# Performance work log

Measured on AMD Instinct MI355X. Metric: run time of the kernel, lower is better.

The kernel has to match this reference:

```python
import jax, jax.numpy as jnp
import numpy as np

N = 50000
E = 400000
NF = 320
HID = 320
EPS = 1e-08


def _linear(x, W, b=None):
    y = x @ W.T
    return y if b is None else y + b


def setup_inputs() -> dict:
    key = jax.random.key(0)
    ks = jax.random.split(key, 16)
    s = 0.05
    inp = {
        "h": jax.random.normal(ks[0], (N, NF), jnp.float32),
        "coord": jax.random.normal(ks[1], (N, 3), jnp.float32),
        "edge_index": jax.random.randint(ks[2], (2, E), 0, N, jnp.int32),
        # edge_mlp: Linear(2*NF+1 -> HID), SiLU, Linear(HID -> HID), SiLU
        "W_e1": jax.random.normal(ks[3], (HID, 2 * NF + 1), jnp.float32) * s,
        "b_e1": jnp.zeros((HID,), jnp.float32),
        "W_e2": jax.random.normal(ks[4], (HID, HID), jnp.float32) * s,
        "b_e2": jnp.zeros((HID,), jnp.float32),
        # node_mlp: Linear(HID+NF -> HID), SiLU, Linear(HID -> NF)
        "W_n1": jax.random.normal(ks[5], (HID, HID + NF), jnp.float32) * s,
        "b_n1": jnp.zeros((HID,), jnp.float32),
        "W_n2": jax.random.normal(ks[6], (NF, HID), jnp.float32) * s,
        "b_n2": jnp.zeros((NF,), jnp.float32),
        # coord_mlp: Linear(HID -> HID), SiLU, Linear(HID -> 1, no bias, xavier gain .001)
        "W_c1": jax.random.normal(ks[7], (HID, HID), jnp.float32) * s,
        "b_c1": jnp.zeros((HID,), jnp.float32),
        "W_c2": jax.random.normal(ks[8], (1, HID), jnp.float32) * 0.001,
    }
    return inp


def reference(h, coord, edge_index, W_e1, b_e1, W_e2, b_e2,
              W_n1, b_n1, W_n2, b_n2, W_c1, b_c1, W_c2):
    row, col = edge_index[0], edge_index[1]

    # coord2radial (normalize=True hard-coded in the module)
    coord_diff = coord[row] - coord[col]                      # [E,3]
    radial = jnp.sum(coord_diff ** 2, axis=1, keepdims=True)  # [E,1]
    norm = jax.lax.stop_gradient(jnp.sqrt(radial)) + EPS
    coord_diff = coord_diff / norm

    # edge model: gather endpoint feats, MLP with SiLU
    edge_in = jnp.concatenate([h[row], h[col], radial], axis=1)   # [E, 2*NF+1]
    m = jax.nn.silu(_linear(edge_in, W_e1, b_e1))
    m = jax.nn.silu(_linear(m, W_e2, b_e2))                       # [E, HID]

    # coord model: per-edge scalar weight, scatter-sum to nodes
    w = _linear(jax.nn.silu(_linear(m, W_c1, b_c1)), W_c2)        # [E,1]
    trans = coord_diff * w                                        # [E,3]
    coord_agg = jax.ops.segment_sum(trans, row, num_segments=N)   # [N,3]
    coord_out = coord + coord_agg

    # node model: scatter-sum messages, MLP, residual
    agg = jax.ops.segment_sum(m, row, num_segments=N)             # [N,HID]
    node_in = jnp.concatenate([h, agg], axis=1)                   # [N,HID+NF]
    out = _linear(jax.nn.silu(_linear(node_in, W_n1, b_n1)), W_n2, b_n2)
    h_out = h + out

    return (h_out, coord_out)
```

## Files before the change

### kernel.cpp

```cpp
#include <hip/hip_runtime.h>

#define NN 50000
#define NE 400000
#define NFD 320
#define NB1 196

typedef short bf16x8 __attribute__((ext_vector_type(8)));
typedef float f32x4 __attribute__((ext_vector_type(4)));

#define MFMA16 __builtin_amdgcn_mfma_f32_16x16x32_bf16

__device__ __forceinline__ unsigned short f2bf(float f){
  unsigned int u = __float_as_uint(f);
  u += 0x7fffu + ((u >> 16) & 1u);
  return (unsigned short)(u >> 16);
}
__device__ __forceinline__ unsigned int cvt_pk_bf16(float lo, float hi){
  unsigned int r;
  asm("v_cvt_pk_bf16_f32 %0, %1, %2" : "=v"(r) : "v"(lo), "v"(hi));
  return r;
}
__device__ __forceinline__ float bflo(unsigned int q){ return __uint_as_float(q << 16); }
__device__ __forceinline__ float bfhi(unsigned int q){ return __uint_as_float(q & 0xffff0000u); }
__device__ __forceinline__ float rcp_fast(float x){
  float r;
  asm("v_rcp_f32 %0, %1" : "=v"(r) : "v"(x));
  return r;
}
__device__ __forceinline__ float silu_f(float x){
  return x * rcp_fast(1.f + __expf(-x));
}

__device__ __forceinline__ void pack_w_body(const float* __restrict__ W,
                                            unsigned short* __restrict__ P,
                                            int kstride, int KS, int idx){
  if (idx >= 20 * KS * 64) return;
  int lane = idx & 63;
  int t  = idx >> 6;
  int ks = t % KS;
  int ct = t / KS;
  const float* src = W + (size_t)(ct*16 + (lane & 15)) * kstride + ks*32 + 8*(lane >> 4);
  unsigned int q[4];
  #pragma unroll
  for (int j = 0; j < 4; j++) q[j] = cvt_pk_bf16(src[2*j], src[2*j+1]);
  *(uint4*)(P + (size_t)idx * 8) = make_uint4(q[0], q[1], q[2], q[3]);
}

__device__ __forceinline__ void pack_stack_body(const float* __restrict__ We1,
                                                unsigned short* __restrict__ P, int idx){
  if (idx >= 40 * 10 * 64) return;
  int lane = idx & 63;
  int t  = idx >> 6;
  int ks = t % 10;
  int ct = t / 10;
  int o  = ct*16 + (lane & 15);
  int k  = ks*32 + 8*(lane >> 4);
  const float* src = (o < 320) ? (We1 + (size_t)o * 641 + k)
                               : (We1 + (size_t)(o - 320) * 641 + 320 + k);
  unsigned int q[4];
  #pragma unroll
  for (int j = 0; j < 4; j++) q[j] = cvt_pk_bf16(src[2*j], src[2*j+1]);
  *(uint4*)(P + (size_t)idx * 8) = make_uint4(q[0], q[1], q[2], q[3]);
}

__global__ void pack_all(const float* __restrict__ We2, const float* __restrict__ Wc1,
                         const float* __restrict__ Wn1, const float* __restrict__ Wn2,
                         const float* __restrict__ We1,
                         unsigned short* __restrict__ We2p, unsigned short* __restrict__ Wc1p,
                         unsigned short* __restrict__ Wn1p, unsigned short* __restrict__ Wn2p,
                         unsigned short* __restrict__ Wsp, float* __restrict__ we1l){
  int b = blockIdx.x;
  int tid = threadIdx.x;
  if (b < 50)       pack_w_body(We2, We2p, 320, 10, b*256 + tid);
  else if (b < 100) pack_w_body(Wc1, Wc1p, 320, 10, (b-50)*256 + tid);
  else if (b < 200) pack_w_body(Wn1, Wn1p, 640, 20, (b-100)*256 + tid);
  else if (b < 250) pack_w_body(Wn2, Wn2p, 320, 10, (b-200)*256 + tid);
  else if (b < 350) pack_stack_body(We1, Wsp, (b-250)*256 + tid);
  else {
    int o = (b - 350)*256 + tid;
    if (o < 320) we1l[o] = We1[(size_t)o * 641 + 640];
  }
}

__global__ void cinit(const float* __restrict__ coord, float* __restrict__ outc){
  int i = blockIdx.x * 256 + threadIdx.x;
  if (i < NN*3) outc[i] = coord[i];
}

__global__ void hist_k(const int* __restrict__ ei, int* __restrict__ cnt){
  int e = blockIdx.x * 256 + threadIdx.x;
  if (e < NE) atomicAdd(&cnt[ei[e]], 1);
}

__global__ void scan1(const int* __restrict__ cnt, int* __restrict__ cur,
                      int* __restrict__ bsum){
  __shared__ int sh[256];
  int tid = threadIdx.x;
  int i = blockIdx.x * 256 + tid;
  int v = (i < NN) ? cnt[i] : 0;
  sh[tid] = v;
  __syncthreads();
  for (int d = 1; d < 256; d <<= 1){
    int u = (tid >= d) ? sh[tid - d] : 0;
    __syncthreads();
    sh[tid] += u;
    __syncthreads();
  }
  if (i < NN) cur[i] = sh[tid] - v;
  if (tid == 255) bsum[blockIdx.x] = sh[255];
}

__global__ void scan2(int* __restrict__ bsum){
  __shared__ int sh[256];
  int tid = threadIdx.x;
  int v = (tid < NB1) ? bsum[tid] : 0;
  sh[tid] = v;
  __syncthreads();
  for (int d = 1; d < 256; d <<= 1){
    int u = (tid >= d) ? sh[tid - d] : 0;
    __syncthreads();
    sh[tid] += u;
    __syncthreads();
  }
  if (tid < NB1) bsum[tid] = sh[tid] - v;
}

__global__ void scan3(int* __restrict__ cur, const int* __restrict__ bsum){
  int i = blockIdx.x * 256 + threadIdx.x;
  if (i < NN) cur[i] += bsum[blockIdx.x];
}

__global__ void scatter_k(const int* __restrict__ ei, int* __restrict__ cur,
                          int* __restrict__ perm){
  int e = blockIdx.x * 256 + threadIdx.x;
  if (e < NE){
    int p = atomicAdd(&cur[ei[e]], 1);
    perm[p] = e;
  }
}

__device__ __forceinline__ void gemm5(const unsigned short* __restrict__ s,
                                      const unsigned short* __restrict__ wp,
                                      int arow0, int arow1, int kl,
                                      int chbase, int lane, f32x4 (&acc)[2][5]){
  const unsigned short* wl0 = wp + (size_t)chbase * 512 + (size_t)lane * 8;
  bf16x8 b0[5], b1[5];
  #pragma unroll
  for (int t = 0; t < 5; t++) b0[t] = *(const bf16x8*)(wl0 + (t*10 + 0)*512);
  #pragma unroll
  for (int t = 0; t < 5; t++) b1[t] = *(const bf16x8*)(wl0 + (t*10 + 1)*512);
  #pragma unroll
  for (int ks = 0; ks < 10; ks++){
    bf16x8 a0 = *(const bf16x8*)(s + arow0*328 + ks*32 + kl);
    bf16x8 a1 = *(const bf16x8*)(s + arow1*328 + ks*32 + kl);
    bf16x8 cur[5];
    #pragma unroll
    for (int t = 0; t < 5; t++) cur[t] = (ks & 1) ? b1[t] : b0[t];
    if (ks < 8){
      #pragma unroll
      for (int t = 0; t < 5; t++){
        bf16x8 nv = *(const bf16x8*)(wl0 + (t*10 + ks + 2)*512);
        if (ks & 1) b1[t] = nv; else b0[t] = nv;
      }
    }
    #pragma unroll
    for (int t = 0; t < 5; t++){
      acc[0][t] = MFMA16(a0, cur[t], acc[0][t], 0, 0, 0);
      acc[1][t] = MFMA16(a1, cur[t], acc[1][t], 0, 0, 0);
    }
  }
}

__device__ __forceinline__ void gemm10(const unsigned short* __restrict__ s,
                                       const unsigned short* __restrict__ wp,
                                       int arow, int kl, int tbase, int kst,
                                       int ksoff, int lane, f32x4 (&acc)[10]){
  const unsigned short* wl0 = wp + (size_t)lane * 8;
  bf16x8 b0[10], b1[10];
  #pragma unroll
  for (int t = 0; t < 10; t++) b0[t] = *(const bf16x8*)(wl0 + (size_t)((tbase+t)*kst + ksoff)*512);
  #pragma unroll
  for (int t = 0; t < 10; t++) b1[t] = *(const bf16x8*)(wl0 + (size_t)((tbase+t)*kst + ksoff + 1)*512);
  #pragma unroll
  for (int ks = 0; ks < 10; ks++){
    bf16x8 a = *(const bf16x8*)(s + arow*328 + ks*32 + kl);
    bf16x8 cur[10];
    #pragma unroll
    for (int t = 0; t < 10; t++) cur[t] = (ks & 1) ? b1[t] : b0[t];
    if (ks < 8){
      #pragma unroll
      for (int t = 0; t < 10; t++){
        bf16x8 nv = *(const bf16x8*)(wl0 + (size_t)((tbase+t)*kst + ksoff + ks + 2)*512);
        if (ks & 1) b1[t] = nv; else b0[t] = nv;
      }
    }
    #pragma unroll
    for (int t = 0; t < 10; t++)
      acc[t] = MFMA16(a, cur[t], acc[t], 0, 0, 0);
  }
}

__global__ void __launch_bounds__(512, 4)
pre_gemm(const float* __restrict__ h, const unsigned short* __restrict__ Wsp,
         const float* __restrict__ be1, unsigned short* __restrict__ P){
  __shared__ __align__(16) unsigned short s_h[32*328];

  const int tid  = threadIdx.x;
  const int lane = tid & 63;
  const int ch   = tid >> 6;
  const int n0   = blockIdx.x * 32;

  const int arow0 = (lane & 15);
  const int arow1 = 16 + (lane & 15);
  const int kl = 8 * (lane >> 4);
  const int rb = (lane >> 4) * 4;

  #pragma unroll
  for (int i = 0; i < 5; i++){
    int idx = tid + i*512;
    int r = idx / 80;
    int c = idx - r*80;
    int node = n0 + r;
    float4 v = (node < NN) ? *(const float4*)(h + (size_t)node*NFD + c*4)
                           : make_float4(0,0,0,0);
    *(uint2*)(s_h + r*328 + c*4) = make_uint2(cvt_pk_bf16(v.x, v.y), cvt_pk_bf16(v.z, v.w));
  }
  __syncthreads();

  f32x4 acc[2][5];
  #pragma unroll
  for (int rt = 0; rt < 2; rt++)
    #pragma unroll
    for (int t = 0; t < 5; t++) acc[rt][t] = {0.f,0.f,0.f,0.f};

  gemm5(s_h, Wsp, arow0, arow1, kl, ch*50, lane, acc);

  #pragma unroll
  for (int rt = 0; rt < 2; rt++){
    #pragma unroll
    for (int t = 0; t < 5; t++){
      int o = (ch*5 + t)*16 + (lane & 15);
      float bb = (o < 320) ? be1[o] : 0.f;
      #pragma unroll
      for (int r = 0; r < 4; r++){
        int node = n0 + rt*16 + rb + r;
        if (node < NN) P[(size_t)node*640 + o] = f2bf(acc[rt][t][r] + bb);
      }
    }
  }
}

__global__ void __launch_bounds__(256, 5)
edge_kernel(const unsigned short* __restrict__ Pbf, const float* __restrict__ coord,
            const int* __restrict__ ei, const int* __restrict__ perm,
            const float* __restrict__ we1l,
            const unsigned short* __restrict__ We2p, const float* __restrict__ be2,
            const unsigned short* __restrict__ Wc1p, const float* __restrict__ bc1,
            const float* __restrict__ Wc2,
            unsigned short* __restrict__ agg, float* __restrict__ cacc)
{
  __shared__ __align__(16) unsigned short s_b[32*328];
  __shared__ float4 s_cd[32];
  __shared__ int s_row[32];
  __shared__ int s_col[32];
  __shared__ float s_w[32];

  const int tid  = threadIdx.x;
  const int lane = tid & 63;
  const int ch   = tid >> 6;
  const int e0   = blockIdx.x * 32;

  if (tid < 32){
    int e = perm[e0 + tid];
    int r = ei[e];
    int c = ei[NE + e];
    s_row[tid] = r; s_col[tid] = c;
    s_w[tid] = 0.f;
    float dx = coord[r*3+0] - coord[c*3+0];
    float dy = coord[r*3+1] - coord[c*3+1];
    float dz = coord[r*3+2] - coord[c*3+2];
    float rad = dx*dx + dy*dy + dz*dz;
    float inv = 1.f / (sqrtf(rad) + 1e-8f);
    s_cd[tid] = make_float4(dx*inv, dy*inv, dz*inv, rad);
  }
  __syncthreads();

  const int arow0 = (lane & 15);
  const int arow1 = 16 + (lane & 15);
  const int kl = 8 * (lane >> 4);
  const int rb = (lane >> 4) * 4;

  #pragma unroll
  for (int i = 0; i < 5; i++){
    int idx = tid + i*256;
    int r = idx / 40;
    int c = idx - r*40;
    uint4 pr = *(const uint4*)(Pbf + (size_t)s_row[r]*640 + c*8);
    uint4 pc = *(const uint4*)(Pbf + (size_t)s_col[r]*640 + 320 + c*8);
    float4 wA = *(const float4*)(we1l + c*8);
    float4 wB = *(const float4*)(we1l + c*8 + 4);
    float rad = s_cd[r].w;
    float v0 = silu_f(bflo(pr.x) + bflo(pc.x) + rad*wA.x);
    float v1 = silu_f(bfhi(pr.x) + bfhi(pc.x) + rad*wA.y);
    float v2 = silu_f(bflo(pr.y) + bflo(pc.y) + rad*wA.z);
    float v3 = silu_f(bfhi(pr.y) + bfhi(pc.y) + rad*wA.w);
    float v4 = silu_f(bflo(pr.z) + bflo(pc.z) + rad*wB.x);
    float v5 = silu_f(bfhi(pr.z) + bfhi(pc.z) + rad*wB.y);
    float v6 = silu_f(bflo(pr.w) + bflo(pc.w) + rad*wB.z);
    float v7 = silu_f(bfhi(pr.w) + bfhi(pc.w) + rad*wB.w);
    uint4 q;
    q.x = cvt_pk_bf16(v0, v1);
    q.y = cvt_pk_bf16(v2, v3);
    q.z = cvt_pk_bf16(v4, v5);
    q.w = cvt_pk_bf16(v6, v7);
    *(uint4*)(s_b + r*328 + c*8) = q;
  }
  __syncthreads();

  f32x4 acc[2][5];

  #pragma unroll
  for (int rt = 0; rt < 2; rt++)
    #pragma unroll
    for (int t = 0; t < 5; t++) acc[rt][t] = {0.f,0.f,0.f,0.f};
  gemm5(s_b, We2p, arow0, arow1, kl, ch*50, lane, acc);
  __syncthreads();
  #pragma unroll
  for (int t = 0; t < 5; t++){
    int o = (ch*5 + t)*16 + (lane & 15);
    float bb = be2[o];
    #pragma unroll
    for (int r = 0; r < 4; r++){
      float v0 = silu_f(acc[0][t][r] + bb);
      float v1 = silu_f(acc[1][t][r] + bb);
      unsigned int q = cvt_pk_bf16(v0, v1);
      int er = rb + r;
      s_b[er*328 + o] = (unsigned short)q;
      s_b[(er+16)*328 + o] = (unsigned short)(q >> 16);
    }
  }
  __syncthreads();

  #pragma unroll
  for (int rt = 0; rt < 2; rt++)
    #pragma unroll
    for (int t = 0; t < 5; t++) acc[rt][t] = {0.f,0.f,0.f,0.f};
  gemm5(s_b, Wc1p, arow0, arow1, kl, ch*50, lane, acc);
  {
    float part[2][4];
    #pragma unroll
    for (int rt = 0; rt < 2; rt++)
      #pragma unroll
      for (int r = 0; r < 4; r++) part[rt][r] = 0.f;
    #pragma unroll
    for (int t = 0; t < 5; t++){
      int o = (ch*5 + t)*16 + (lane & 15);
      float bb = bc1[o];
      float wc = Wc2[o];
      #pragma unroll
      for (int rt = 0; rt < 2; rt++)
        #pragma unroll
        for (int r = 0; r < 4; r++)
          part[rt][r] = fmaf(silu_f(acc[rt][t][r] + bb), wc, part[rt][r]);
    }
    #pragma unroll
    for (int rt = 0; rt < 2; rt++)
      #pragma unroll
      for (int r = 0; r < 4; r++){
        float p = part[rt][r];
        p += __shfl_xor(p, 1);
        p += __shfl_xor(p, 2);
        p += __shfl_xor(p, 4);
        p += __shfl_xor(p, 8);
        if ((lane & 15) == 0)
          atomicAdd(&s_w[rt*16 + (lane >> 4)*4 + r], p);
      }
  }
  __syncthreads();

  if (tid < 160){
    int p = tid;
    float a0 = 0.f, a1 = 0.f;
    #pragma unroll
    for (int e = 0; e < 32; e++){
      unsigned int q = *(const unsigned int*)(s_b + e*328 + p*2);
      a0 += bflo(q); a1 += bfhi(q);
      if (e == 31 || s_row[e+1] != s_row[e]){
        unsigned int val = cvt_pk_bf16(a0, a1);
        unsigned short* dst = agg + (size_t)s_row[e]*NFD + p*2;
        asm volatile("global_atomic_pk_add_bf16 %0, %1, off" :: "v"(dst), "v"(val) : "memory");
        a0 = 0.f; a1 = 0.f;
      }
    }
  }
  if (tid >= 192 && tid < 195){
    int d = tid - 192;
    float a = 0.f;
    #pragma unroll
    for (int e = 0; e < 32; e++){
      float cdc = (d == 0) ? s_cd[e].x : (d == 1) ? s_cd[e].y : s_cd[e].z;
      a += cdc * s_w[e];
      if (e == 31 || s_row[e+1] != s_row[e]){
        atomicAdd(cacc + (size_t)s_row[e]*3 + d, a);
        a = 0.f;
      }
    }
  }
}

__global__ void __launch_bounds__(256, 4)
node_kernel(const float* __restrict__ h, const unsigned short* __restrict__ agg,
            const unsigned short* __restrict__ Wn1p, const float* __restrict__ bn1,
            const unsigned short* __restrict__ Wn2p, const float* __restrict__ bn2,
            float* __restrict__ hout)
{
  __shared__ __align__(16) unsigned short s_b[32*328];

  const int tid  = threadIdx.x;
  const int lane = tid & 63;
  const int wv   = tid >> 6;
  const int n0   = blockIdx.x * 32;

  const int rt = wv & 1;
  const int ch = wv >> 1;
  const int arow = rt*16 + (lane & 15);
  const int kl = 8 * (lane >> 4);
  const int colbase = ch * 160;
  const int rbase = rt*16 + (lane >> 4)*4;

  f32x4 acc[10];
  #pragma unroll
  for (int t = 0; t < 10; t++) acc[t] = {0.f,0.f,0.f,0.f};

  #pragma unroll
  for (int i = 0; i < 10; i++){
    int idx = tid + i*256;
    int r = idx / 80;
    int c = idx - r*80;
    int node = n0 + r;
    float4 v = (node < NN) ? *(const float4*)(h + (size_t)node*NFD + c*4)
                           : make_float4(0,0,0,0);
    *(uint2*)(s_b + r*328 + c*4) = make_uint2(cvt_pk_bf16(v.x, v.y), cvt_pk_bf16(v.z, v.w));
  }
  __syncthreads();

  gemm10(s_b, Wn1p, arow, kl, ch*10, 20, 0, lane, acc);
  __syncthreads();

  #pragma unroll
  for (int i = 0; i < 5; i++){
    int idx = tid + i*256;
    int r = idx / 40;
    int c = idx - r*40;
    int node = n0 + r;
    uint4 v = (node < NN) ? *(const uint4*)(agg + (size_t)node*NFD + c*8)
                          : make_uint4(0,0,0,0);
    *(uint4*)(s_b + r*328 + c*8) = v;
  }
  __syncthreads();

  gemm10(s_b, Wn1p, arow, kl, ch*10, 20, 10, lane, acc);
  __syncthreads();

  #pragma unroll
  for (int t = 0; t < 10; t++){
    int o = colbase + t*16 + (lane & 15);
    float bb = bn1[o];
    #pragma unroll
    for (int r = 0; r < 4; r++)
      s_b[(rbase + r)*328 + o] = f2bf(silu_f(acc[t][r] + bb));
  }
  __syncthreads();

  #pragma unroll
  for (int t = 0; t < 10; t++) acc[t] = {0.f,0.f,0.f,0.f};
  gemm10(s_b, Wn2p, arow, kl, ch*10, 10, 0, lane, acc);
  #pragma unroll
  for (int t = 0; t < 10; t++){
    int o = colbase + t*16 + (lane & 15);
    float bb = bn2[o];
    #pragma unroll
    for (int r = 0; r < 4; r++){
      int node = n0 + rbase + r;
      if (node < NN)
        hout[(size_t)node*NFD + o] = h[(size_t)node*NFD + o] + acc[t][r] + bb;
    }
  }
}

extern "C" void kernel_launch(void* const* d_in, const int* in_sizes, int n_in,
                              void* d_out, int out_size, void* d_ws, size_t ws_size,
                              hipStream_t stream){
  const float* h     = (const float*)d_in[0];
  const float* coord = (const float*)d_in[1];
  const int*   ei    = (const int*)d_in[2];
  const float* We1 = (const float*)d_in[3];
  const float* be1 = (const float*)d_in[4];
  const float* We2 = (const float*)d_in[5];
  const float* be2 = (const float*)d_in[6];
  const float* Wn1 = (const float*)d_in[7];
  const float* bn1 = (const float*)d_in[8];
  const float* Wn2 = (const float*)d_in[9];
  const float* bn2 = (const float*)d_in[10];
  const float* Wc1 = (const float*)d_in[11];
  const float* bc1 = (const float*)d_in[12];
  const float* Wc2 = (const float*)d_in[13];

  char* ws = (char*)d_ws;
  unsigned short* We2p = (unsigned short*)(ws);
  unsigned short* Wc1p = (unsigned short*)(ws + 204800);
  unsigned short* Wn1p = (unsigned short*)(ws + 409600);
  unsigned short* Wn2p = (unsigned short*)(ws + 819200);
  unsigned short* Wsp  = (unsigned short*)(ws + 1024000);
  float*          we1l = (float*)(ws + 1433600);
  unsigned short* agg  = (unsigned short*)(ws + 1434880);
  int*            cnt  = (int*)(ws + 33434880);
  int*            cur  = (int*)(ws + 33634880);
  int*            perm = (int*)(ws + 33834880);
  int*            bsum = (int*)(ws + 35434880);

  float* hout = (float*)d_out;
  float* cout = hout + (size_t)NN * NFD;
  unsigned short* Pbf = (unsigned short*)d_out;

  hipMemsetAsync(agg, 0, (size_t)NN * NFD * 2, stream);
  hipMemsetAsync(cnt, 0, (size_t)NN * 4, stream);

  cinit<<<(NN*3 + 255)/256, 256, 0, stream>>>(coord, cout);

  pack_all<<<352, 256, 0, stream>>>(We2, Wc1, Wn1, Wn2, We1,
                                    We2p, Wc1p, Wn1p, Wn2p, Wsp, we1l);

  hist_k<<<(NE + 255)/256, 256, 0, stream>>>(ei, cnt);
  scan1<<<NB1, 256, 0, stream>>>(cnt, cur, bsum);
  scan2<<<1, 256, 0, stream>>>(bsum);
  scan3<<<NB1, 256, 0, stream>>>(cur, bsum);
  scatter_k<<<(NE + 255)/256, 256, 0, stream>>>(ei, cur, perm);

  pre_gemm<<<(NN + 31)/32, 512, 0, stream>>>(h, Wsp, be1, Pbf);

  edge_kernel<<<NE/32, 256, 0, stream>>>(Pbf, coord, ei, perm, we1l,
                                         We2p, be2, Wc1p, bc1, Wc2, agg, cout);
  node_kernel<<<(NN + 31)/32, 256, 0, stream>>>(h, agg, Wn1p, bn1, Wn2p, bn2, hout);
}
```

Before: 559.3 us.

## Merge coord init with histogram, retile node kernel to 2x5 MFMA tiles, tweak bounds

Fuses the coord-copy and edge histogram kernels into one launch to drop a kernel launch. Rewrites node_kernel so each wave computes two 16-row tiles by five 16-column tiles via a generalized gemm5 with a stride parameter, reusing each loaded weight fragment across two row tiles instead of one. Launch-bound occupancy hints change for pre_gemm, edge_kernel and node_kernel, which alters register budgets and may cause spills.

```diff
diff --git a/kernel.cpp b/kernel.cpp
--- a/kernel.cpp
+++ b/kernel.cpp
@@ -4,6 +4,7 @@
 #define NE 400000
 #define NFD 320
 #define NB1 196
+#define CB  587
 
 typedef short bf16x8 __attribute__((ext_vector_type(8)));
 typedef float f32x4 __attribute__((ext_vector_type(4)));
@@ -82,14 +83,16 @@
   }
 }
 
-__global__ void cinit(const float* __restrict__ coord, float* __restrict__ outc){
-  int i = blockIdx.x * 256 + threadIdx.x;
-  if (i < NN*3) outc[i] = coord[i];
-}
-
-__global__ void hist_k(const int* __restrict__ ei, int* __restrict__ cnt){
-  int e = blockIdx.x * 256 + threadIdx.x;
-  if (e < NE) atomicAdd(&cnt[ei[e]], 1);
+__global__ void init_hist(const float* __restrict__ coord, float* __restrict__ outc,
+                          const int* __restrict__ ei, int* __restrict__ cnt){
+  int b = blockIdx.x;
+  if (b < CB){
+    int i = b * 256 + threadIdx.x;
+    if (i < NN*3) outc[i] = coord[i];
+  } else {
+    int e = (b - CB) * 256 + threadIdx.x;
+    if (e < NE) atomicAdd(&cnt[ei[e]], 1);
+  }
 }
 
 __global__ void scan1(const int* __restrict__ cnt, int* __restrict__ cur,
@@ -142,13 +145,13 @@
 __device__ __forceinline__ void gemm5(const unsigned short* __restrict__ s,
                                       const unsigned short* __restrict__ wp,
                                       int arow0, int arow1, int kl,
-                                      int chbase, int lane, f32x4 (&acc)[2][5]){
-  const unsigned short* wl0 = wp + (size_t)chbase * 512 + (size_t)lane * 8;
+                                      int fragbase, int KST, int lane, f32x4 (&acc)[2][5]){
+  const unsigned short* wl0 = wp + (size_t)fragbase * 512 + (size_t)lane * 8;
   bf16x8 b0[5], b1[5];
   #pragma unroll
-  for (int t = 0; t < 5; t++) b0[t] = *(const bf16x8*)(wl0 + (t*10 + 0)*512);
-  #pragma unroll
-  for (int t = 0; t < 5; t++) b1[t] = *(const bf16x8*)(wl0 + (t*10 + 1)*512);
+  for (int t = 0; t < 5; t++) b0[t] = *(const bf16x8*)(wl0 + (t*KST + 0)*512);
+  #pragma unroll
+  for (int t = 0; t < 5; t++) b1[t] = *(const bf16x8*)(wl0 + (t*KST + 1)*512);
   #pragma unroll
   for (int ks = 0; ks < 10; ks++){
     bf16x8 a0 = *(const bf16x8*)(s + arow0*328 + ks*32 + kl);
@@ -159,7 +162,7 @@
     if (ks < 8){
       #pragma unroll
       for (int t = 0; t < 5; t++){
-        bf16x8 nv = *(const bf16x8*)(wl0 + (t*10 + ks + 2)*512);
+        bf16x8 nv = *(const bf16x8*)(wl0 + (t*KST + ks + 2)*512);
         if (ks & 1) b1[t] = nv; else b0[t] = nv;
       }
     }
@@ -171,36 +174,7 @@
   }
 }
 
-__device__ __forceinline__ void gemm10(const unsigned short* __restrict__ s,
-                                       const unsigned short* __restrict__ wp,
-                                       int arow, int kl, int tbase, int kst,
-                                       int ksoff, int lane, f32x4 (&acc)[10]){
-  const unsigned short* wl0 = wp + (size_t)lane * 8;
-  bf16x8 b0[10], b1[10];
-  #pragma unroll
-  for (int t = 0; t < 10; t++) b0[t] = *(const bf16x8*)(wl0 + (size_t)((tbase+t)*kst + ksoff)*512);
-  #pragma unroll
-  for (int t = 0; t < 10; t++) b1[t] = *(const bf16x8*)(wl0 + (size_t)((tbase+t)*kst + ksoff + 1)*512);
-  #pragma unroll
-  for (int ks = 0; ks < 10; ks++){
-    bf16x8 a = *(const bf16x8*)(s + arow*328 + ks*32 + kl);
-    bf16x8 cur[10];
-    #pragma unroll
-    for (int t = 0; t < 10; t++) cur[t] = (ks & 1) ? b1[t] : b0[t];
-    if (ks < 8){
-      #pragma unroll
-      for (int t = 0; t < 10; t++){
-        bf16x8 nv = *(const bf16x8*)(wl0 + (size_t)((tbase+t)*kst + ksoff + ks + 2)*512);
-        if (ks & 1) b1[t] = nv; else b0[t] = nv;
-      }
-    }
-    #pragma unroll
-    for (int t = 0; t < 10; t++)
-      acc[t] = MFMA16(a, cur[t], acc[t], 0, 0, 0);
-  }
-}
-
-__global__ void __launch_bounds__(512, 4)
+__global__ void __launch_bounds__(512, 2)
 pre_gemm(const float* __restrict__ h, const unsigned short* __restrict__ Wsp,
          const float* __restrict__ be1, unsigned short* __restrict__ P){
   __shared__ __align__(16) unsigned short s_h[32*328];
@@ -233,7 +207,7 @@
     #pragma unroll
     for (int t = 0; t < 5; t++) acc[rt][t] = {0.f,0.f,0.f,0.f};
 
-  gemm5(s_h, Wsp, arow0, arow1, kl, ch*50, lane, acc);
+  gemm5(s_h, Wsp, arow0, arow1, kl, ch*50, 10, lane, acc);
 
   #pragma unroll
   for (int rt = 0; rt < 2; rt++){
@@ -250,7 +224,7 @@
   }
 }
 
-__global__ void __launch_bounds__(256, 5)
+__global__ void __launch_bounds__(256, 6)
 edge_kernel(const unsigned short* __restrict__ Pbf, const float* __restrict__ coord,
             const int* __restrict__ ei, const int* __restrict__ perm,
             const float* __restrict__ we1l,
@@ -323,7 +297,7 @@
   for (int rt = 0; rt < 2; rt++)
     #pragma unroll
     for (int t = 0; t < 5; t++) acc[rt][t] = {0.f,0.f,0.f,0.f};
-  gemm5(s_b, We2p, arow0, arow1, kl, ch*50, lane, acc);
+  gemm5(s_b, We2p, arow0, arow1, kl, ch*50, 10, lane, acc);
   __syncthreads();
   #pragma unroll
   for (int t = 0; t < 5; t++){
@@ -345,7 +319,7 @@
   for (int rt = 0; rt < 2; rt++)
     #pragma unroll
     for (int t = 0; t < 5; t++) acc[rt][t] = {0.f,0.f,0.f,0.f};
-  gemm5(s_b, Wc1p, arow0, arow1, kl, ch*50, lane, acc);
+  gemm5(s_b, Wc1p, arow0, arow1, kl, ch*50, 10, lane, acc);
   {
     float part[2][4];
     #pragma unroll
@@ -408,7 +382,7 @@
   }
 }
 
-__global__ void __launch_bounds__(256, 4)
+__global__ void __launch_bounds__(256, 5)
 node_kernel(const float* __restrict__ h, const unsigned short* __restrict__ agg,
             const unsigned short* __restrict__ Wn1p, const float* __restrict__ bn1,
             const unsigned short* __restrict__ Wn2p, const float* __restrict__ bn2,
@@ -418,19 +392,19 @@
 
   const int tid  = threadIdx.x;
   const int lane = tid & 63;
-  const int wv   = tid >> 6;
+  const int ch   = tid >> 6;
   const int n0   = blockIdx.x * 32;
 
-  const int rt = wv & 1;
-  const int ch = wv >> 1;
-  const int arow = rt*16 + (lane & 15);
+  const int arow0 = (lane & 15);
+  const int arow1 = 16 + (lane & 15);
   const int kl = 8 * (lane >> 4);
-  const int colbase = ch * 160;
-  const int rbase = rt*16 + (lane >> 4)*4;
-
-  f32x4 acc[10];
-  #pragma unroll
-  for (int t = 0; t < 10; t++) acc[t] = {0.f,0.f,0.f,0.f};
+  const int rb = (lane >> 4) * 4;
+
+  f32x4 acc[2][5];
+  #pragma unroll
+  for (int rt = 0; rt < 2; rt++)
+    #pragma unroll
+    for (int t = 0; t < 5; t++) acc[rt][t] = {0.f,0.f,0.f,0.f};
 
   #pragma unroll
   for (int i = 0; i < 10; i++){
@@ -444,7 +418,7 @@
   }
   __syncthreads();
 
-  gemm10(s_b, Wn1p, arow, kl, ch*10, 20, 0, lane, acc);
+  gemm5(s_b, Wn1p, arow0, arow1, kl, ch*100, 20, lane, acc);
   __syncthreads();
 
   #pragma unroll
@@ -459,31 +433,42 @@
   }
   __syncthreads();
 
-  gemm10(s_b, Wn1p, arow, kl, ch*10, 20, 10, lane, acc);
-  __syncthreads();
-
-  #pragma unroll
-  for (int t = 0; t < 10; t++){
-    int o = colbase + t*16 + (lane & 15);
+  gemm5(s_b, Wn1p, arow0, arow1, kl, ch*100 + 10, 20, lane, acc);
+  __syncthreads();
+
+  #pragma unroll
+  for (int t = 0; t < 5; t++){
+    int o = (ch*5 + t)*16 + (lane & 15);
     float bb = bn1[o];
     #pragma unroll
-    for (int r = 0; r < 4; r++)
-      s_b[(rbase + r)*328 + o] = f2bf(silu_f(acc[t][r] + bb));
-  }
-  __syncthreads();
-
-  #pragma unroll
-  for (int t = 0; t < 10; t++) acc[t] = {0.f,0.f,0.f,0.f};
-  gemm10(s_b, Wn2p, arow, kl, ch*10, 10, 0, lane, acc);
-  #pragma unroll
-  for (int t = 0; t < 10; t++){
-    int o = colbase + t*16 + (lane & 15);
+    for (int r = 0; r < 4; r++){
+      float v0 = silu_f(acc[0][t][r] + bb);
+      float v1 = silu_f(acc[1][t][r] + bb);
+      unsigned int q = cvt_pk_bf16(v0, v1);
+      int er = rb + r;
+      s_b[er*328 + o] = (unsigned short)q;
+      s_b[(er+16)*328 + o] = (unsigned short)(q >> 16);
+    }
+  }
+  __syncthreads();
+
+  #pragma unroll
+  for (int rt = 0; rt < 2; rt++)
+    #pragma unroll
+    for (int t = 0; t < 5; t++) acc[rt][t] = {0.f,0.f,0.f,0.f};
+  gemm5(s_b, Wn2p, arow0, arow1, kl, ch*50, 10, lane, acc);
+  #pragma unroll
+  for (int t = 0; t < 5; t++){
+    int o = (ch*5 + t)*16 + (lane & 15);
     float bb = bn2[o];
     #pragma unroll
     for (int r = 0; r < 4; r++){
-      int node = n0 + rbase + r;
-      if (node < NN)
-        hout[(size_t)node*NFD + o] = h[(size_t)node*NFD + o] + acc[t][r] + bb;
+      int node0 = n0 + rb + r;
+      int node1 = node0 + 16;
+      if (node0 < NN)
+        hout[(size_t)node0*NFD + o] = h[(size_t)node0*NFD + o] + acc[0][t][r] + bb;
+      if (node1 < NN)
+        hout[(size_t)node1*NFD + o] = h[(size_t)node1*NFD + o] + acc[1][t][r] + bb;
     }
   }
 }
@@ -526,12 +511,10 @@
   hipMemsetAsync(agg, 0, (size_t)NN * NFD * 2, stream);
   hipMemsetAsync(cnt, 0, (size_t)NN * 4, stream);
 
-  cinit<<<(NN*3 + 255)/256, 256, 0, stream>>>(coord, cout);
-
   pack_all<<<352, 256, 0, stream>>>(We2, Wc1, Wn1, Wn2, We1,
                                     We2p, Wc1p, Wn1p, Wn2p, Wsp, we1l);
 
-  hist_k<<<(NE + 255)/256, 256, 0, stream>>>(ei, cnt);
+  init_hist<<<CB + (NE + 255)/256, 256, 0, stream>>>(coord, cout, ei, cnt);
   scan1<<<NB1, 256, 0, stream>>>(cnt, cur, bsum);
   scan2<<<1, 256, 0, stream>>>(bsum);
   scan3<<<NB1, 256, 0, stream>>>(cur, bsum);
```

Measured after the change: 579.8 us. 3.7% more time.
